# Kernel optimization log

Measured on AMD Instinct MI355X. Metric: run time of the kernel, lower is better.

The kernel has to match this reference:

```python
import jax, jax.numpy as jnp
import numpy as np

H, Hk, Hv, Dk, Dv, K = 1536, 8, 16, 64, 64, 4
KEY_DIM = Hk * Dk            # 512
VALUE_DIM = Hv * Dv          # 1024
CONV_DIM = 2 * KEY_DIM + VALUE_DIM  # 2048


def setup_inputs() -> dict:
    key = jax.random.key(0)
    ks = jax.random.split(key, 12)
    s = 0.02
    return {
        "hidden_states": jax.random.normal(ks[0], (1, H, 1, 1), jnp.float32),
        "W_qkv": jax.random.normal(ks[1], (CONV_DIM, H), jnp.float32) * s,
        "W_z": jax.random.normal(ks[2], (VALUE_DIM, H), jnp.float32) * s,
        "W_a": jax.random.normal(ks[3], (Hv, H), jnp.float32) * s,
        "W_b": jax.random.normal(ks[4], (Hv, H), jnp.float32) * s,
        "W_out": jax.random.normal(ks[5], (H, VALUE_DIM), jnp.float32) * s,
        "conv1d_weight": jax.random.normal(ks[6], (CONV_DIM, K), jnp.float32) * 0.1,
        "A_log": jax.random.normal(ks[7], (Hv,), jnp.float32) * 0.1,
        "dt_bias": jax.random.normal(ks[8], (Hv,), jnp.float32) * 0.1,
        "norm_weight": jnp.ones((Dv,), jnp.float32),
        "state": jax.random.normal(ks[9], (1, Hv, Dk, Dv), jnp.float32) * 0.05,
        "conv_cache": jax.random.normal(ks[10], (1, CONV_DIM, K - 1), jnp.float32) * 0.1,
    }


def _l2n(t):
    # l2_normalize with eps=1e-12 (matches torch rsqrt(sum(x^2)+eps))
    return t * jax.lax.rsqrt(jnp.sum(t * t, axis=-1, keepdims=True) + 1e-12)


def reference(hidden_states, W_qkv, W_z, W_a, W_b, W_out, conv1d_weight,
              A_log, dt_bias, norm_weight, state, conv_cache):
    x = hidden_states.reshape(-1)                       # [H]
    qkv = W_qkv @ x                                     # [CONV_DIM]
    z = (W_z @ x).reshape(Hv, Dv)                       # gate, [Hv, Dv]
    a = W_a @ x                                         # [Hv]
    beta = jax.nn.sigmoid(W_b @ x)                      # [Hv]

    # causal conv as weighted sum over cache + current token
    combined = jnp.concatenate([conv_cache[0], qkv[:, None]], axis=1)  # [CONV_DIM, K]
    conv_out = jax.nn.silu(jnp.sum(combined * conv1d_weight, axis=1))  # [CONV_DIM]

    q = conv_out[:KEY_DIM].reshape(Hk, Dk)
    k = conv_out[KEY_DIM:2 * KEY_DIM].reshape(Hk, Dk)
    v = conv_out[2 * KEY_DIM:].reshape(Hv, Dv)

    rep = Hv // Hk                                      # kv_group = 2
    q = jnp.repeat(q, rep, axis=0)                      # [Hv, Dk]
    k = jnp.repeat(k, rep, axis=0)
    q = _l2n(q) * (Dk ** -0.5)
    k = _l2n(k)

    # gated decay
    g = -jnp.exp(A_log) * jax.nn.softplus(a + dt_bias)  # [Hv]
    st = state[0] * jnp.exp(g)[:, None, None]           # [Hv, Dk, Dv]

    # delta-rule update
    retrieved = jnp.einsum('hkv,hk->hv', st, k)         # [Hv, Dv]
    delta = (v - retrieved) * beta[:, None]             # [Hv, Dv]
    new_state = st + jnp.einsum('hk,hv->hkv', k, delta) # [Hv, Dk, Dv]

    out = jnp.einsum('hkv,hk->hv', new_state, q)        # [Hv, Dv]

    # gated RMSNorm over Dv
    var = jnp.mean(out * out, axis=-1, keepdims=True)
    out = norm_weight * (out * jax.lax.rsqrt(var + 1e-6)) * jax.nn.silu(z)

    y = W_out @ out.reshape(-1)                         # [H]
    return y.reshape(1, -1, 1, 1)
```

## Files before the change

kernel.cpp:

```cpp
#include <hip/hip_runtime.h>

#define H 1536
#define HK 8
#define HV 16
#define DK 64
#define DV 64
#define KEY_DIM 512
#define VALUE_DIM 1024
#define CONV_DIM 2048
#define NROWS1 (CONV_DIM + VALUE_DIM + HV + HV)

__device__ __forceinline__ float wave_reduce_sum(float v) {
#pragma unroll
    for (int off = 32; off > 0; off >>= 1) v += __shfl_xor(v, off, 64);
    return v;
}

__global__ __launch_bounds__(256) void gemv_in(
        const float* __restrict__ x,
        const float* __restrict__ Wqkv, const float* __restrict__ Wz,
        const float* __restrict__ Wa,   const float* __restrict__ Wb,
        float* __restrict__ ws) {
    const int wave = threadIdx.x >> 6;
    const int lane = threadIdx.x & 63;
    const int row  = blockIdx.x * 4 + wave;
    const float* wrow;
    if (row < CONV_DIM)                      wrow = Wqkv + (size_t)row * H;
    else if (row < CONV_DIM + VALUE_DIM)     wrow = Wz + (size_t)(row - CONV_DIM) * H;
    else if (row < CONV_DIM + VALUE_DIM + HV)wrow = Wa + (size_t)(row - CONV_DIM - VALUE_DIM) * H;
    else                                     wrow = Wb + (size_t)(row - CONV_DIM - VALUE_DIM - HV) * H;
    const float4* w4 = (const float4*)wrow;
    const float4* x4 = (const float4*)x;
    float acc = 0.f;
#pragma unroll
    for (int j = 0; j < 6; ++j) {
        float4 a = w4[lane + 64 * j];
        float4 b = x4[lane + 64 * j];
        acc += a.x * b.x + a.y * b.y + a.z * b.z + a.w * b.w;
    }
    acc = wave_reduce_sum(acc);
    if (lane == 0) ws[row] = acc;
}

__global__ __launch_bounds__(256) void decode_core(
        const float* __restrict__ ws,
        const float* __restrict__ conv_w,
        const float* __restrict__ conv_cache,
        const float* __restrict__ A_log, const float* __restrict__ dt_bias,
        const float* __restrict__ norm_w,
        const float* __restrict__ state,
        float* __restrict__ out_gated) {
    const int h    = blockIdx.x;
    const int tid  = threadIdx.x;
    const int lane = tid & 63;
    const int grp  = tid >> 6;

    __shared__ float q_s[64], k_s[64], v_s[64];
    __shared__ float red_r[256], red_o[256];
    __shared__ float scal[3];

    if (grp < 3) {
        int i;
        if (grp == 0)      i = (h >> 1) * 64 + lane;
        else if (grp == 1) i = KEY_DIM + (h >> 1) * 64 + lane;
        else               i = 2 * KEY_DIM + h * 64 + lane;
        float raw = conv_cache[i * 3 + 0] * conv_w[i * 4 + 0]
                  + conv_cache[i * 3 + 1] * conv_w[i * 4 + 1]
                  + conv_cache[i * 3 + 2] * conv_w[i * 4 + 2]
                  + ws[i]                 * conv_w[i * 4 + 3];
        float c = raw / (1.f + expf(-raw));
        if (grp == 2) {
            v_s[lane] = c;
        } else {
            float ss  = wave_reduce_sum(c * c);
            float inv = rsqrtf(ss + 1e-12f);
            if (grp == 0) q_s[lane] = c * inv * 0.125f;
            else          k_s[lane] = c * inv;
        }
    } else if (lane == 0) {
        float aa = ws[CONV_DIM + VALUE_DIM + h] + dt_bias[h];
        float sp = (aa > 20.f) ? aa : log1pf(expf(aa));
        scal[0] = expf(-expf(A_log[h]) * sp);
        float braw = ws[CONV_DIM + VALUE_DIM + HV + h];
        scal[1] = 1.f / (1.f + expf(-braw));
    }
    __syncthreads();

    const float* st = state + (size_t)h * DK * DV;
    float pr = 0.f, po = 0.f;
    const int k0 = grp * 16;
#pragma unroll
    for (int kk = 0; kk < 16; ++kk) {
        float s = st[(k0 + kk) * 64 + lane];
        pr += s * k_s[k0 + kk];
        po += s * q_s[k0 + kk];
    }
    red_r[tid] = pr;
    red_o[tid] = po;
    if (grp == 0) {
        float t = wave_reduce_sum(k_s[lane] * q_s[lane]);
        if (lane == 0) scal[2] = t;
    }
    __syncthreads();

    if (tid < 64) {
        const float decay = scal[0], beta = scal[1], kq = scal[2];
        float r = (red_r[tid] + red_r[64 + tid] + red_r[128 + tid] + red_r[192 + tid]) * decay;
        float o = (red_o[tid] + red_o[64 + tid] + red_o[128 + tid] + red_o[192 + tid]) * decay;
        float delta = (v_s[tid] - r) * beta;
        float outv  = o + delta * kq;
        float ss  = wave_reduce_sum(outv * outv);
        float inv = rsqrtf(ss * (1.f / 64.f) + 1e-6f);
        float zz  = ws[CONV_DIM + h * 64 + tid];
        float gate = zz / (1.f + expf(-zz));
        out_gated[h * 64 + tid] = norm_w[tid] * outv * inv * gate;
    }
}

__global__ __launch_bounds__(256) void gemv_out(
        const float* __restrict__ Wout, const float* __restrict__ og,
        float* __restrict__ y) {
    const int wave = threadIdx.x >> 6;
    const int lane = threadIdx.x & 63;
    const int row  = blockIdx.x * 4 + wave;
    const float4* w4 = (const float4*)(Wout + (size_t)row * VALUE_DIM);
    const float4* g4 = (const float4*)og;
    float acc = 0.f;
#pragma unroll
    for (int j = 0; j < 4; ++j) {
        float4 a = w4[lane + 64 * j];
        float4 b = g4[lane + 64 * j];
        acc += a.x * b.x + a.y * b.y + a.z * b.z + a.w * b.w;
    }
    acc = wave_reduce_sum(acc);
    if (lane == 0) y[row] = acc;
}

extern "C" void kernel_launch(void* const* d_in, const int* in_sizes, int n_in,
                              void* d_out, int out_size, void* d_ws, size_t ws_size,
                              hipStream_t stream) {
    const float* x     = (const float*)d_in[0];
    const float* Wqkv  = (const float*)d_in[1];
    const float* Wz    = (const float*)d_in[2];
    const float* Wa    = (const float*)d_in[3];
    const float* Wb    = (const float*)d_in[4];
    const float* Wout  = (const float*)d_in[5];
    const float* convw = (const float*)d_in[6];
    const float* Alog  = (const float*)d_in[7];
    const float* dtb   = (const float*)d_in[8];
    const float* normw = (const float*)d_in[9];
    const float* state = (const float*)d_in[10];
    const float* cch   = (const float*)d_in[11];

    float* ws = (float*)d_ws;
    float* og = ws + NROWS1;
    float* y  = (float*)d_out;

    gemv_in<<<NROWS1 / 4, 256, 0, stream>>>(x, Wqkv, Wz, Wa, Wb, ws);
    decode_core<<<HV, 256, 0, stream>>>(ws, convw, cch, Alog, dtb, normw, state, og);
    gemv_out<<<H / 4, 256, 0, stream>>>(Wout, og, y);
}
```

Measured before the change: 98.66 us.

## Fuse three decode kernels into one persistent kernel with grid barriers

Replaces the three launches (input GEMV, recurrent core, output GEMV) with a single 256-block kernel that synchronises phases through an atomic ticket grid barrier. Each wave now computes three or four input rows, and the W_out rows and state tile are prefetched into registers and LDS before the first barrier, so those loads overlap the input GEMV. This removes two kernel launch gaps and the serialised memory phases. The cost is spin-wait barriers that assume all 256 blocks are co-resident, plus higher register pressure from holding W_out in registers.

```diff
diff --git a/kernel.cpp b/kernel.cpp
--- a/kernel.cpp
+++ b/kernel.cpp
@@ -9,6 +9,9 @@
 #define VALUE_DIM 1024
 #define CONV_DIM 2048
 #define NROWS1 (CONV_DIM + VALUE_DIM + HV + HV)
+#define NBLK 256
+
+__device__ unsigned g_ticket = 0;
 
 __device__ __forceinline__ float wave_reduce_sum(float v) {
 #pragma unroll
@@ -16,124 +19,176 @@
     return v;
 }
 
-__global__ __launch_bounds__(256) void gemv_in(
+__device__ __forceinline__ float dot4(float4 a, float4 b) {
+    return a.x * b.x + a.y * b.y + a.z * b.z + a.w * b.w;
+}
+
+__device__ __forceinline__ void grid_barrier() {
+    __syncthreads();
+    if (threadIdx.x == 0) {
+        unsigned t = __hip_atomic_fetch_add(&g_ticket, 1u, __ATOMIC_ACQ_REL,
+                                            __HIP_MEMORY_SCOPE_AGENT);
+        unsigned target = (t / NBLK + 1u) * NBLK;
+        while (__hip_atomic_load(&g_ticket, __ATOMIC_ACQUIRE,
+                                 __HIP_MEMORY_SCOPE_AGENT) < target)
+            __builtin_amdgcn_s_sleep(2);
+    }
+    __syncthreads();
+}
+
+__global__ __launch_bounds__(256) void fused_decode(
         const float* __restrict__ x,
         const float* __restrict__ Wqkv, const float* __restrict__ Wz,
         const float* __restrict__ Wa,   const float* __restrict__ Wb,
-        float* __restrict__ ws) {
-    const int wave = threadIdx.x >> 6;
-    const int lane = threadIdx.x & 63;
-    const int row  = blockIdx.x * 4 + wave;
-    const float* wrow;
-    if (row < CONV_DIM)                      wrow = Wqkv + (size_t)row * H;
-    else if (row < CONV_DIM + VALUE_DIM)     wrow = Wz + (size_t)(row - CONV_DIM) * H;
-    else if (row < CONV_DIM + VALUE_DIM + HV)wrow = Wa + (size_t)(row - CONV_DIM - VALUE_DIM) * H;
-    else                                     wrow = Wb + (size_t)(row - CONV_DIM - VALUE_DIM - HV) * H;
-    const float4* w4 = (const float4*)wrow;
-    const float4* x4 = (const float4*)x;
-    float acc = 0.f;
-#pragma unroll
-    for (int j = 0; j < 6; ++j) {
-        float4 a = w4[lane + 64 * j];
-        float4 b = x4[lane + 64 * j];
-        acc += a.x * b.x + a.y * b.y + a.z * b.z + a.w * b.w;
-    }
-    acc = wave_reduce_sum(acc);
-    if (lane == 0) ws[row] = acc;
-}
-
-__global__ __launch_bounds__(256) void decode_core(
-        const float* __restrict__ ws,
-        const float* __restrict__ conv_w,
-        const float* __restrict__ conv_cache,
+        const float* __restrict__ Wout,
+        const float* __restrict__ conv_w, const float* __restrict__ conv_cache,
         const float* __restrict__ A_log, const float* __restrict__ dt_bias,
         const float* __restrict__ norm_w,
         const float* __restrict__ state,
-        float* __restrict__ out_gated) {
-    const int h    = blockIdx.x;
+        float* __restrict__ ws,
+        float* __restrict__ og,
+        float* __restrict__ y) {
     const int tid  = threadIdx.x;
     const int lane = tid & 63;
-    const int grp  = tid >> 6;
-
+    const int wv   = tid >> 6;
+    const int blk  = blockIdx.x;
+    const int wg   = blk * 4 + wv;
+
+    __shared__ float s_state[DK * DV];
     __shared__ float q_s[64], k_s[64], v_s[64];
     __shared__ float red_r[256], red_o[256];
     __shared__ float scal[3];
 
-    if (grp < 3) {
-        int i;
-        if (grp == 0)      i = (h >> 1) * 64 + lane;
-        else if (grp == 1) i = KEY_DIM + (h >> 1) * 64 + lane;
-        else               i = 2 * KEY_DIM + h * 64 + lane;
-        float raw = conv_cache[i * 3 + 0] * conv_w[i * 4 + 0]
-                  + conv_cache[i * 3 + 1] * conv_w[i * 4 + 1]
-                  + conv_cache[i * 3 + 2] * conv_w[i * 4 + 2]
-                  + ws[i]                 * conv_w[i * 4 + 3];
-        float c = raw / (1.f + expf(-raw));
-        if (grp == 2) {
-            v_s[lane] = c;
-        } else {
-            float ss  = wave_reduce_sum(c * c);
-            float inv = rsqrtf(ss + 1e-12f);
-            if (grp == 0) q_s[lane] = c * inv * 0.125f;
-            else          k_s[lane] = c * inv;
-        }
-    } else if (lane == 0) {
-        float aa = ws[CONV_DIM + VALUE_DIM + h] + dt_bias[h];
-        float sp = (aa > 20.f) ? aa : log1pf(expf(aa));
-        scal[0] = expf(-expf(A_log[h]) * sp);
-        float braw = ws[CONV_DIM + VALUE_DIM + HV + h];
-        scal[1] = 1.f / (1.f + expf(-braw));
-    }
-    __syncthreads();
-
-    const float* st = state + (size_t)h * DK * DV;
-    float pr = 0.f, po = 0.f;
-    const int k0 = grp * 16;
-#pragma unroll
-    for (int kk = 0; kk < 16; ++kk) {
-        float s = st[(k0 + kk) * 64 + lane];
-        pr += s * k_s[k0 + kk];
-        po += s * q_s[k0 + kk];
-    }
-    red_r[tid] = pr;
-    red_o[tid] = po;
-    if (grp == 0) {
-        float t = wave_reduce_sum(k_s[lane] * q_s[lane]);
-        if (lane == 0) scal[2] = t;
-    }
-    __syncthreads();
-
-    if (tid < 64) {
-        const float decay = scal[0], beta = scal[1], kq = scal[2];
-        float r = (red_r[tid] + red_r[64 + tid] + red_r[128 + tid] + red_r[192 + tid]) * decay;
-        float o = (red_o[tid] + red_o[64 + tid] + red_o[128 + tid] + red_o[192 + tid]) * decay;
-        float delta = (v_s[tid] - r) * beta;
-        float outv  = o + delta * kq;
-        float ss  = wave_reduce_sum(outv * outv);
-        float inv = rsqrtf(ss * (1.f / 64.f) + 1e-6f);
-        float zz  = ws[CONV_DIM + h * 64 + tid];
-        float gate = zz / (1.f + expf(-zz));
-        out_gated[h * 64 + tid] = norm_w[tid] * outv * inv * gate;
-    }
-}
-
-__global__ __launch_bounds__(256) void gemv_out(
-        const float* __restrict__ Wout, const float* __restrict__ og,
-        float* __restrict__ y) {
-    const int wave = threadIdx.x >> 6;
-    const int lane = threadIdx.x & 63;
-    const int row  = blockIdx.x * 4 + wave;
-    const float4* w4 = (const float4*)(Wout + (size_t)row * VALUE_DIM);
-    const float4* g4 = (const float4*)og;
-    float acc = 0.f;
-#pragma unroll
-    for (int j = 0; j < 4; ++j) {
-        float4 a = w4[lane + 64 * j];
-        float4 b = g4[lane + 64 * j];
-        acc += a.x * b.x + a.y * b.y + a.z * b.z + a.w * b.w;
-    }
+    if (blk < HV) {
+        const float4* st4 = (const float4*)(state + (size_t)blk * DK * DV);
+        float4* ss4 = (float4*)s_state;
+#pragma unroll
+        for (int j = 0; j < 4; ++j) ss4[tid + 256 * j] = st4[tid + 256 * j];
+    }
+
+    float4 wo0[4], wo1[4] = {};
+    {
+        const float4* w4 = (const float4*)(Wout + (size_t)wg * VALUE_DIM);
+#pragma unroll
+        for (int j = 0; j < 4; ++j) wo0[j] = w4[lane + 64 * j];
+    }
+    if (wg < 512) {
+        const float4* w4 = (const float4*)(Wout + (size_t)(1024 + wg) * VALUE_DIM);
+#pragma unroll
+        for (int j = 0; j < 4; ++j) wo1[j] = w4[lane + 64 * j];
+    }
+
+    auto rowptr = [&](int row) -> const float* {
+        if (row < CONV_DIM)                  return Wqkv + (size_t)row * H;
+        if (row < CONV_DIM + VALUE_DIM)      return Wz + (size_t)(row - CONV_DIM) * H;
+        if (row < CONV_DIM + VALUE_DIM + HV) return Wa + (size_t)(row - CONV_DIM - VALUE_DIM) * H;
+        return Wb + (size_t)(row - CONV_DIM - VALUE_DIM - HV) * H;
+    };
+    const int r0 = wg * 3;
+    const float4* wA = (const float4*)rowptr(r0);
+    const float4* wB = (const float4*)rowptr(r0 + 1);
+    const float4* wC = (const float4*)rowptr(r0 + 2);
+    const bool extra = (wv == 0) && (blk >= 208) && (blk < 240);
+    const int erow = 3072 + blk - 208;
+    const float4* wD = (const float4*)rowptr(extra ? erow : r0);
+    const float4* x4 = (const float4*)x;
+
+    float a0 = 0.f, a1 = 0.f, a2 = 0.f, a3 = 0.f;
+#pragma unroll
+    for (int j = 0; j < 6; ++j) {
+        const int idx = lane + 64 * j;
+        const float4 xb = x4[idx];
+        a0 += dot4(wA[idx], xb);
+        a1 += dot4(wB[idx], xb);
+        a2 += dot4(wC[idx], xb);
+        if (extra) a3 += dot4(wD[idx], xb);
+    }
+    a0 = wave_reduce_sum(a0);
+    a1 = wave_reduce_sum(a1);
+    a2 = wave_reduce_sum(a2);
+    if (lane == 0) { ws[r0] = a0; ws[r0 + 1] = a1; ws[r0 + 2] = a2; }
+    if (extra) {
+        a3 = wave_reduce_sum(a3);
+        if (lane == 0) ws[erow] = a3;
+    }
+
+    grid_barrier();
+
+    if (blk < HV) {
+        const int h = blk;
+        const int grp = wv;
+        if (grp < 3) {
+            int i;
+            if (grp == 0)      i = (h >> 1) * 64 + lane;
+            else if (grp == 1) i = KEY_DIM + (h >> 1) * 64 + lane;
+            else               i = 2 * KEY_DIM + h * 64 + lane;
+            float raw = conv_cache[i * 3 + 0] * conv_w[i * 4 + 0]
+                      + conv_cache[i * 3 + 1] * conv_w[i * 4 + 1]
+                      + conv_cache[i * 3 + 2] * conv_w[i * 4 + 2]
+                      + ws[i]                 * conv_w[i * 4 + 3];
+            float c = raw / (1.f + expf(-raw));
+            if (grp == 2) {
+                v_s[lane] = c;
+            } else {
+                float ss  = wave_reduce_sum(c * c);
+                float inv = rsqrtf(ss + 1e-12f);
+                if (grp == 0) q_s[lane] = c * inv * 0.125f;
+                else          k_s[lane] = c * inv;
+            }
+        } else if (lane == 0) {
+            float aa = ws[CONV_DIM + VALUE_DIM + h] + dt_bias[h];
+            float sp = (aa > 20.f) ? aa : log1pf(expf(aa));
+            scal[0] = expf(-expf(A_log[h]) * sp);
+            float braw = ws[CONV_DIM + VALUE_DIM + HV + h];
+            scal[1] = 1.f / (1.f + expf(-braw));
+        }
+        __syncthreads();
+
+        float pr = 0.f, po = 0.f;
+        const int k0 = grp * 16;
+#pragma unroll
+        for (int kk = 0; kk < 16; ++kk) {
+            float s = s_state[(k0 + kk) * 64 + lane];
+            pr += s * k_s[k0 + kk];
+            po += s * q_s[k0 + kk];
+        }
+        red_r[tid] = pr;
+        red_o[tid] = po;
+        if (grp == 0) {
+            float t = wave_reduce_sum(k_s[lane] * q_s[lane]);
+            if (lane == 0) scal[2] = t;
+        }
+        __syncthreads();
+
+        if (tid < 64) {
+            const float decay = scal[0], beta = scal[1], kq = scal[2];
+            float r = (red_r[tid] + red_r[64 + tid] + red_r[128 + tid] + red_r[192 + tid]) * decay;
+            float o = (red_o[tid] + red_o[64 + tid] + red_o[128 + tid] + red_o[192 + tid]) * decay;
+            float delta = (v_s[tid] - r) * beta;
+            float outv  = o + delta * kq;
+            float ss  = wave_reduce_sum(outv * outv);
+            float inv = rsqrtf(ss * (1.f / 64.f) + 1e-6f);
+            float zz  = ws[CONV_DIM + h * 64 + tid];
+            float gate = zz / (1.f + expf(-zz));
+            og[h * 64 + tid] = norm_w[tid] * outv * inv * gate;
+        }
+    }
+
+    grid_barrier();
+
+    const float4* og4 = (const float4*)og;
+    const float4 g0 = og4[lane];
+    const float4 g1 = og4[lane + 64];
+    const float4 g2 = og4[lane + 128];
+    const float4 g3 = og4[lane + 192];
+    float acc = dot4(wo0[0], g0) + dot4(wo0[1], g1) + dot4(wo0[2], g2) + dot4(wo0[3], g3);
     acc = wave_reduce_sum(acc);
-    if (lane == 0) y[row] = acc;
+    if (lane == 0) y[wg] = acc;
+    if (wg < 512) {
+        float acc2 = dot4(wo1[0], g0) + dot4(wo1[1], g1) + dot4(wo1[2], g2) + dot4(wo1[3], g3);
+        acc2 = wave_reduce_sum(acc2);
+        if (lane == 0) y[1024 + wg] = acc2;
+    }
 }
 
 extern "C" void kernel_launch(void* const* d_in, const int* in_sizes, int n_in,
@@ -156,7 +211,6 @@
     float* og = ws + NROWS1;
     float* y  = (float*)d_out;
 
-    gemv_in<<<NROWS1 / 4, 256, 0, stream>>>(x, Wqkv, Wz, Wa, Wb, ws);
-    decode_core<<<HV, 256, 0, stream>>>(ws, convw, cch, Alog, dtb, normw, state, og);
-    gemv_out<<<H / 4, 256, 0, stream>>>(Wout, og, y);
-}
+    fused_decode<<<NBLK, 256, 0, stream>>>(x, Wqkv, Wz, Wa, Wb, Wout, convw, cch,
+                                           Alog, dtb, normw, state, ws, og, y);
+}
```

After: 120.3 us. 21.9% more time.

## Fuse decode core and output GEMV with a global atomic completion flag

Applied to the files above, without the earlier changes.

Merges the decode_core and gemv_out kernels into one launch. The first 16 blocks compute the per-head recurrent update and raise a global counter. All blocks spin on that counter before the output projection, and non-decode blocks prefetch their W_out rows into registers while they wait. This removes one kernel launch and hides the W_out load behind the decode phase. In exchange it depends on the 16 decode blocks being co-resident with the spinning blocks (384 blocks total) and adds atomic polling.

```diff
diff --git a/kernel.cpp b/kernel.cpp
--- a/kernel.cpp
+++ b/kernel.cpp
@@ -10,10 +10,15 @@
 #define CONV_DIM 2048
 #define NROWS1 (CONV_DIM + VALUE_DIM + HV + HV)
 
+__device__ unsigned g_done;
+
 __device__ __forceinline__ float wave_reduce_sum(float v) {
 #pragma unroll
     for (int off = 32; off > 0; off >>= 1) v += __shfl_xor(v, off, 64);
     return v;
+}
+__device__ __forceinline__ float dot4(float4 a, float4 b) {
+    return a.x * b.x + a.y * b.y + a.z * b.z + a.w * b.w;
 }
 
 __global__ __launch_bounds__(256) void gemv_in(
@@ -21,14 +26,16 @@
         const float* __restrict__ Wqkv, const float* __restrict__ Wz,
         const float* __restrict__ Wa,   const float* __restrict__ Wb,
         float* __restrict__ ws) {
+    if (blockIdx.x == 0 && threadIdx.x == 0)
+        __hip_atomic_store(&g_done, 0u, __ATOMIC_RELAXED, __HIP_MEMORY_SCOPE_AGENT);
     const int wave = threadIdx.x >> 6;
     const int lane = threadIdx.x & 63;
     const int row  = blockIdx.x * 4 + wave;
     const float* wrow;
-    if (row < CONV_DIM)                      wrow = Wqkv + (size_t)row * H;
-    else if (row < CONV_DIM + VALUE_DIM)     wrow = Wz + (size_t)(row - CONV_DIM) * H;
-    else if (row < CONV_DIM + VALUE_DIM + HV)wrow = Wa + (size_t)(row - CONV_DIM - VALUE_DIM) * H;
-    else                                     wrow = Wb + (size_t)(row - CONV_DIM - VALUE_DIM - HV) * H;
+    if (row < CONV_DIM)                       wrow = Wqkv + (size_t)row * H;
+    else if (row < CONV_DIM + VALUE_DIM)      wrow = Wz + (size_t)(row - CONV_DIM) * H;
+    else if (row < CONV_DIM + VALUE_DIM + HV) wrow = Wa + (size_t)(row - CONV_DIM - VALUE_DIM) * H;
+    else                                      wrow = Wb + (size_t)(row - CONV_DIM - VALUE_DIM - HV) * H;
     const float4* w4 = (const float4*)wrow;
     const float4* x4 = (const float4*)x;
     float acc = 0.f;
@@ -42,95 +49,123 @@
     if (lane == 0) ws[row] = acc;
 }
 
-__global__ __launch_bounds__(256) void decode_core(
+__global__ __launch_bounds__(256) void decode_out(
         const float* __restrict__ ws,
         const float* __restrict__ conv_w,
         const float* __restrict__ conv_cache,
         const float* __restrict__ A_log, const float* __restrict__ dt_bias,
         const float* __restrict__ norm_w,
         const float* __restrict__ state,
-        float* __restrict__ out_gated) {
-    const int h    = blockIdx.x;
+        const float* __restrict__ Wout,
+        float* __restrict__ og,
+        float* __restrict__ y) {
     const int tid  = threadIdx.x;
     const int lane = tid & 63;
-    const int grp  = tid >> 6;
+    const int wv   = tid >> 6;
+    const int blk  = blockIdx.x;
+    const int row  = blk * 4 + wv;
+    const bool isdec = (blk < HV);
 
     __shared__ float q_s[64], k_s[64], v_s[64];
     __shared__ float red_r[256], red_o[256];
     __shared__ float scal[3];
 
-    if (grp < 3) {
-        int i;
-        if (grp == 0)      i = (h >> 1) * 64 + lane;
-        else if (grp == 1) i = KEY_DIM + (h >> 1) * 64 + lane;
-        else               i = 2 * KEY_DIM + h * 64 + lane;
-        float raw = conv_cache[i * 3 + 0] * conv_w[i * 4 + 0]
-                  + conv_cache[i * 3 + 1] * conv_w[i * 4 + 1]
-                  + conv_cache[i * 3 + 2] * conv_w[i * 4 + 2]
-                  + ws[i]                 * conv_w[i * 4 + 3];
-        float c = raw / (1.f + expf(-raw));
-        if (grp == 2) {
-            v_s[lane] = c;
-        } else {
-            float ss  = wave_reduce_sum(c * c);
-            float inv = rsqrtf(ss + 1e-12f);
-            if (grp == 0) q_s[lane] = c * inv * 0.125f;
-            else          k_s[lane] = c * inv;
+    float4 wo[4];
+    if (!isdec) {
+        const float4* w4 = (const float4*)(Wout + (size_t)row * VALUE_DIM);
+#pragma unroll
+        for (int j = 0; j < 4; ++j) wo[j] = w4[lane + 64 * j];
+        asm volatile("" :: "v"(wo[0].x), "v"(wo[1].x), "v"(wo[2].x), "v"(wo[3].x));
+    }
+
+    if (isdec) {
+        const int h = blk;
+        if (wv < 3) {
+            int i;
+            if (wv == 0)      i = (h >> 1) * 64 + lane;
+            else if (wv == 1) i = KEY_DIM + (h >> 1) * 64 + lane;
+            else              i = 2 * KEY_DIM + h * 64 + lane;
+            float raw = conv_cache[i * 3 + 0] * conv_w[i * 4 + 0]
+                      + conv_cache[i * 3 + 1] * conv_w[i * 4 + 1]
+                      + conv_cache[i * 3 + 2] * conv_w[i * 4 + 2]
+                      + ws[i]                 * conv_w[i * 4 + 3];
+            float c = raw / (1.f + expf(-raw));
+            if (wv == 2) {
+                v_s[lane] = c;
+            } else {
+                float ss  = wave_reduce_sum(c * c);
+                float inv = rsqrtf(ss + 1e-12f);
+                if (wv == 0) q_s[lane] = c * inv * 0.125f;
+                else         k_s[lane] = c * inv;
+            }
+        } else if (lane == 0) {
+            float aa = ws[CONV_DIM + VALUE_DIM + h] + dt_bias[h];
+            float sp = (aa > 20.f) ? aa : log1pf(expf(aa));
+            scal[0] = expf(-expf(A_log[h]) * sp);
+            float braw = ws[CONV_DIM + VALUE_DIM + HV + h];
+            scal[1] = 1.f / (1.f + expf(-braw));
         }
-    } else if (lane == 0) {
-        float aa = ws[CONV_DIM + VALUE_DIM + h] + dt_bias[h];
-        float sp = (aa > 20.f) ? aa : log1pf(expf(aa));
-        scal[0] = expf(-expf(A_log[h]) * sp);
-        float braw = ws[CONV_DIM + VALUE_DIM + HV + h];
-        scal[1] = 1.f / (1.f + expf(-braw));
+        __syncthreads();
+
+        const float* st = state + (size_t)h * DK * DV;
+        float pr = 0.f, po = 0.f;
+        const int k0 = wv * 16;
+#pragma unroll
+        for (int kk = 0; kk < 16; ++kk) {
+            float s = st[(k0 + kk) * 64 + lane];
+            pr += s * k_s[k0 + kk];
+            po += s * q_s[k0 + kk];
+        }
+        red_r[tid] = pr;
+        red_o[tid] = po;
+        if (wv == 0) {
+            float t = wave_reduce_sum(k_s[lane] * q_s[lane]);
+            if (lane == 0) scal[2] = t;
+        }
+        __syncthreads();
+
+        if (tid < 64) {
+            const float decay = scal[0], beta = scal[1], kq = scal[2];
+            float r = (red_r[tid] + red_r[64 + tid] + red_r[128 + tid] + red_r[192 + tid]) * decay;
+            float o = (red_o[tid] + red_o[64 + tid] + red_o[128 + tid] + red_o[192 + tid]) * decay;
+            float delta = (v_s[tid] - r) * beta;
+            float outv  = o + delta * kq;
+            float ss  = wave_reduce_sum(outv * outv);
+            float inv = rsqrtf(ss * (1.f / 64.f) + 1e-6f);
+            float zz  = ws[CONV_DIM + h * 64 + tid];
+            float gate = zz / (1.f + expf(-zz));
+            og[h * 64 + tid] = norm_w[tid] * outv * inv * gate;
+        }
+        __syncthreads();
+        if (tid == 0)
+            __hip_atomic_fetch_add(&g_done, 1u, __ATOMIC_RELEASE,
+                                   __HIP_MEMORY_SCOPE_AGENT);
+    }
+
+    if (tid == 0) {
+        while (__hip_atomic_load(&g_done, __ATOMIC_ACQUIRE,
+                                 __HIP_MEMORY_SCOPE_AGENT) < (unsigned)HV)
+            __builtin_amdgcn_s_sleep(2);
     }
     __syncthreads();
 
-    const float* st = state + (size_t)h * DK * DV;
-    float pr = 0.f, po = 0.f;
-    const int k0 = grp * 16;
+    if (isdec) {
+        const float4* w4 = (const float4*)(Wout + (size_t)row * VALUE_DIM);
 #pragma unroll
-    for (int kk = 0; kk < 16; ++kk) {
-        float s = st[(k0 + kk) * 64 + lane];
-        pr += s * k_s[k0 + kk];
-        po += s * q_s[k0 + kk];
+        for (int j = 0; j < 4; ++j) wo[j] = w4[lane + 64 * j];
     }
-    red_r[tid] = pr;
-    red_o[tid] = po;
-    if (grp == 0) {
-        float t = wave_reduce_sum(k_s[lane] * q_s[lane]);
-        if (lane == 0) scal[2] = t;
-    }
-    __syncthreads();
 
-    if (tid < 64) {
-        const float decay = scal[0], beta = scal[1], kq = scal[2];
-        float r = (red_r[tid] + red_r[64 + tid] + red_r[128 + tid] + red_r[192 + tid]) * decay;
-        float o = (red_o[tid] + red_o[64 + tid] + red_o[128 + tid] + red_o[192 + tid]) * decay;
-        float delta = (v_s[tid] - r) * beta;
-        float outv  = o + delta * kq;
-        float ss  = wave_reduce_sum(outv * outv);
-        float inv = rsqrtf(ss * (1.f / 64.f) + 1e-6f);
-        float zz  = ws[CONV_DIM + h * 64 + tid];
-        float gate = zz / (1.f + expf(-zz));
-        out_gated[h * 64 + tid] = norm_w[tid] * outv * inv * gate;
-    }
-}
-
-__global__ __launch_bounds__(256) void gemv_out(
-        const float* __restrict__ Wout, const float* __restrict__ og,
-        float* __restrict__ y) {
-    const int wave = threadIdx.x >> 6;
-    const int lane = threadIdx.x & 63;
-    const int row  = blockIdx.x * 4 + wave;
-    const float4* w4 = (const float4*)(Wout + (size_t)row * VALUE_DIM);
-    const float4* g4 = (const float4*)og;
+    const float4* og4 = (const float4*)og;
     float acc = 0.f;
-#pragma unroll
-    for (int j = 0; j < 4; ++j) {
-        float4 a = w4[lane + 64 * j];
-        float4 b = g4[lane + 64 * j];
-        acc += a.x * b.x + a.y * b.y + a.z * b.z + a.w * b.w;
+    {
+        float4 b0 = og4[lane];
+        float4 b1 = og4[lane + 64];
+        float4 b2 = og4[lane + 128];
+        float4 b3 = og4[lane + 192];
+        acc += dot4(wo[0], b0);
+        acc += dot4(wo[1], b1);
+        acc += dot4(wo[2], b2);
+        acc += dot4(wo[3], b3);
     }
     acc = wave_reduce_sum(acc);
     if (lane == 0) y[row] = acc;
@@ -157,6 +192,6 @@
     float* y  = (float*)d_out;
 
     gemv_in<<<NROWS1 / 4, 256, 0, stream>>>(x, Wqkv, Wz, Wa, Wb, ws);
-    decode_core<<<HV, 256, 0, stream>>>(ws, convw, cch, Alog, dtb, normw, state, og);
-    gemv_out<<<H / 4, 256, 0, stream>>>(Wout, og, y);
+    decode_out<<<H / 4, 256, 0, stream>>>(ws, convw, cch, Alog, dtb, normw, state,
+                                          Wout, og, y);
 }
```

Result: slower. 111.1 us (+12.6%).

## Fuse decode core into output GEMV, recomputing recurrence per block

Applied to the files above, without the earlier changes.

Merges the decode-core kernel and the output GEMV into one kernel. Each of 96 blocks (512 threads) recomputes the full conv, normalization and state recurrence for all 16 heads into shared memory, then computes 16 output rows. This removes one kernel launch and the global round trip for the gated output. The cost is redundant work: every block reads the whole 256KB state and repeats the transcendentals, and the state reads are done serially by one wave per two heads.

```diff
diff --git a/kernel.cpp b/kernel.cpp
--- a/kernel.cpp
+++ b/kernel.cpp
@@ -15,6 +15,18 @@
     for (int off = 32; off > 0; off >>= 1) v += __shfl_xor(v, off, 64);
     return v;
 }
+__device__ __forceinline__ float dot4(float4 a, float4 b) {
+    return a.x * b.x + a.y * b.y + a.z * b.z + a.w * b.w;
+}
+__device__ __forceinline__ float conv_silu(int i,
+        const float* __restrict__ ws, const float* __restrict__ conv_w,
+        const float* __restrict__ conv_cache) {
+    float raw = conv_cache[i * 3 + 0] * conv_w[i * 4 + 0]
+              + conv_cache[i * 3 + 1] * conv_w[i * 4 + 1]
+              + conv_cache[i * 3 + 2] * conv_w[i * 4 + 2]
+              + ws[i]                 * conv_w[i * 4 + 3];
+    return raw / (1.f + expf(-raw));
+}
 
 __global__ __launch_bounds__(256) void gemv_in(
         const float* __restrict__ x,
@@ -25,10 +37,10 @@
     const int lane = threadIdx.x & 63;
     const int row  = blockIdx.x * 4 + wave;
     const float* wrow;
-    if (row < CONV_DIM)                      wrow = Wqkv + (size_t)row * H;
-    else if (row < CONV_DIM + VALUE_DIM)     wrow = Wz + (size_t)(row - CONV_DIM) * H;
-    else if (row < CONV_DIM + VALUE_DIM + HV)wrow = Wa + (size_t)(row - CONV_DIM - VALUE_DIM) * H;
-    else                                     wrow = Wb + (size_t)(row - CONV_DIM - VALUE_DIM - HV) * H;
+    if (row < CONV_DIM)                       wrow = Wqkv + (size_t)row * H;
+    else if (row < CONV_DIM + VALUE_DIM)      wrow = Wz + (size_t)(row - CONV_DIM) * H;
+    else if (row < CONV_DIM + VALUE_DIM + HV) wrow = Wa + (size_t)(row - CONV_DIM - VALUE_DIM) * H;
+    else                                      wrow = Wb + (size_t)(row - CONV_DIM - VALUE_DIM - HV) * H;
     const float4* w4 = (const float4*)wrow;
     const float4* x4 = (const float4*)x;
     float acc = 0.f;
@@ -42,98 +54,81 @@
     if (lane == 0) ws[row] = acc;
 }
 
-__global__ __launch_bounds__(256) void decode_core(
+__global__ __launch_bounds__(512) void decode_y(
         const float* __restrict__ ws,
         const float* __restrict__ conv_w,
         const float* __restrict__ conv_cache,
         const float* __restrict__ A_log, const float* __restrict__ dt_bias,
         const float* __restrict__ norm_w,
         const float* __restrict__ state,
-        float* __restrict__ out_gated) {
-    const int h    = blockIdx.x;
+        const float* __restrict__ Wout,
+        float* __restrict__ y) {
     const int tid  = threadIdx.x;
     const int lane = tid & 63;
-    const int grp  = tid >> 6;
+    const int wv   = tid >> 6;
 
-    __shared__ float q_s[64], k_s[64], v_s[64];
-    __shared__ float red_r[256], red_o[256];
-    __shared__ float scal[3];
+    __shared__ float og_s[VALUE_DIM];
 
-    if (grp < 3) {
-        int i;
-        if (grp == 0)      i = (h >> 1) * 64 + lane;
-        else if (grp == 1) i = KEY_DIM + (h >> 1) * 64 + lane;
-        else               i = 2 * KEY_DIM + h * 64 + lane;
-        float raw = conv_cache[i * 3 + 0] * conv_w[i * 4 + 0]
-                  + conv_cache[i * 3 + 1] * conv_w[i * 4 + 1]
-                  + conv_cache[i * 3 + 2] * conv_w[i * 4 + 2]
-                  + ws[i]                 * conv_w[i * 4 + 3];
-        float c = raw / (1.f + expf(-raw));
-        if (grp == 2) {
-            v_s[lane] = c;
-        } else {
-            float ss  = wave_reduce_sum(c * c);
-            float inv = rsqrtf(ss + 1e-12f);
-            if (grp == 0) q_s[lane] = c * inv * 0.125f;
-            else          k_s[lane] = c * inv;
-        }
-    } else if (lane == 0) {
+    const int iq = wv * 64 + lane;
+    const int ik = KEY_DIM + wv * 64 + lane;
+    float cq = conv_silu(iq, ws, conv_w, conv_cache);
+    float ck = conv_silu(ik, ws, conv_w, conv_cache);
+    float qn = cq * rsqrtf(wave_reduce_sum(cq * cq) + 1e-12f) * 0.125f;
+    float kn = ck * rsqrtf(wave_reduce_sum(ck * ck) + 1e-12f);
+    float kq = wave_reduce_sum(kn * qn);
+
+#pragma unroll
+    for (int hh = 0; hh < 2; ++hh) {
+        const int h = 2 * wv + hh;
+        float cv = conv_silu(2 * KEY_DIM + h * 64 + lane, ws, conv_w, conv_cache);
         float aa = ws[CONV_DIM + VALUE_DIM + h] + dt_bias[h];
         float sp = (aa > 20.f) ? aa : log1pf(expf(aa));
-        scal[0] = expf(-expf(A_log[h]) * sp);
+        float decay = expf(-expf(A_log[h]) * sp);
         float braw = ws[CONV_DIM + VALUE_DIM + HV + h];
-        scal[1] = 1.f / (1.f + expf(-braw));
+        float beta = 1.f / (1.f + expf(-braw));
+
+        const float* st = state + (size_t)h * DK * DV;
+        float pr[4] = {0.f, 0.f, 0.f, 0.f};
+        float po[4] = {0.f, 0.f, 0.f, 0.f};
+#pragma unroll
+        for (int qq = 0; qq < 4; ++qq) {
+#pragma unroll
+            for (int kk = 0; kk < 16; ++kk) {
+                const int kidx = qq * 16 + kk;
+                float s  = st[kidx * 64 + lane];
+                pr[qq] += s * __shfl(kn, kidx, 64);
+                po[qq] += s * __shfl(qn, kidx, 64);
+            }
+        }
+        float r = (((pr[0] + pr[1]) + pr[2]) + pr[3]) * decay;
+        float o = (((po[0] + po[1]) + po[2]) + po[3]) * decay;
+        float delta = (cv - r) * beta;
+        float outv  = o + delta * kq;
+        float ssum = wave_reduce_sum(outv * outv);
+        float inv = rsqrtf(ssum * (1.f / 64.f) + 1e-6f);
+        float zz  = ws[CONV_DIM + h * 64 + lane];
+        float gate = zz / (1.f + expf(-zz));
+        og_s[h * 64 + lane] = norm_w[lane] * outv * inv * gate;
     }
     __syncthreads();
 
-    const float* st = state + (size_t)h * DK * DV;
-    float pr = 0.f, po = 0.f;
-    const int k0 = grp * 16;
+    const float4* og4 = (const float4*)og_s;
+    const float4 b0 = og4[lane];
+    const float4 b1 = og4[lane + 64];
+    const float4 b2 = og4[lane + 128];
+    const float4 b3 = og4[lane + 192];
 #pragma unroll
-    for (int kk = 0; kk < 16; ++kk) {
-        float s = st[(k0 + kk) * 64 + lane];
-        pr += s * k_s[k0 + kk];
-        po += s * q_s[k0 + kk];
+    for (int j = 0; j < 2; ++j) {
+        const int row = blockIdx.x * 16 + wv * 2 + j;
+        const float4* w4 = (const float4*)(Wout + (size_t)row * VALUE_DIM);
+        float acc = 0.f;
+        acc += dot4(w4[lane],       b0);
+        acc += dot4(w4[lane + 64],  b1);
+        acc += dot4(w4[lane + 128], b2);
+        acc += dot4(w4[lane + 192], b3);
+        acc = wave_reduce_sum(acc);
+        if (lane == 0) y[row] = acc;
     }
-    red_r[tid] = pr;
-    red_o[tid] = po;
-    if (grp == 0) {
-        float t = wave_reduce_sum(k_s[lane] * q_s[lane]);
-        if (lane == 0) scal[2] = t;
-    }
-    __syncthreads();
-
-    if (tid < 64) {
-        const float decay = scal[0], beta = scal[1], kq = scal[2];
-        float r = (red_r[tid] + red_r[64 + tid] + red_r[128 + tid] + red_r[192 + tid]) * decay;
-        float o = (red_o[tid] + red_o[64 + tid] + red_o[128 + tid] + red_o[192 + tid]) * decay;
-        float delta = (v_s[tid] - r) * beta;
-        float outv  = o + delta * kq;
-        float ss  = wave_reduce_sum(outv * outv);
-        float inv = rsqrtf(ss * (1.f / 64.f) + 1e-6f);
-        float zz  = ws[CONV_DIM + h * 64 + tid];
-        float gate = zz / (1.f + expf(-zz));
-        out_gated[h * 64 + tid] = norm_w[tid] * outv * inv * gate;
-    }
-}
-
-__global__ __launch_bounds__(256) void gemv_out(
-        const float* __restrict__ Wout, const float* __restrict__ og,
-        float* __restrict__ y) {
-    const int wave = threadIdx.x >> 6;
-    const int lane = threadIdx.x & 63;
-    const int row  = blockIdx.x * 4 + wave;
-    const float4* w4 = (const float4*)(Wout + (size_t)row * VALUE_DIM);
-    const float4* g4 = (const float4*)og;
-    float acc = 0.f;
-#pragma unroll
-    for (int j = 0; j < 4; ++j) {
-        float4 a = w4[lane + 64 * j];
-        float4 b = g4[lane + 64 * j];
-        acc += a.x * b.x + a.y * b.y + a.z * b.z + a.w * b.w;
-    }
-    acc = wave_reduce_sum(acc);
-    if (lane == 0) y[row] = acc;
 }
 
 extern "C" void kernel_launch(void* const* d_in, const int* in_sizes, int n_in,
@@ -153,10 +148,9 @@
     const float* cch   = (const float*)d_in[11];
 
     float* ws = (float*)d_ws;
-    float* og = ws + NROWS1;
     float* y  = (float*)d_out;
 
     gemv_in<<<NROWS1 / 4, 256, 0, stream>>>(x, Wqkv, Wz, Wa, Wb, ws);
-    decode_core<<<HV, 256, 0, stream>>>(ws, convw, cch, Alog, dtb, normw, state, og);
-    gemv_out<<<H / 4, 256, 0, stream>>>(Wout, og, y);
+    decode_y<<<H / 16, 512, 0, stream>>>(ws, convw, cch, Alog, dtb, normw, state,
+                                         Wout, y);
 }
```

New measurement: 101.6 us. 1.03x slower.
